# Kernel optimization log

Hardware: AMD Instinct MI355X
Metric: run time of the kernel (lower is better)

## Reference

```python
import jax, jax.numpy as jnp
import numpy as np

H = 256      # hidden_size
IN = 128     # lstm input_size
A = 64       # attention_features
F = 1024     # vocab_features
V = 50000    # vocab_size
S = 512      # src_len
T = 32       # dec_len
B = 32       # batch


def _lstm_layer(x, h0, c0, Wih, Whh, bih, bhh):
    # x: [T,B,in]; PyTorch gate order i,f,g,o
    def step(carry, xt):
        h, c = carry
        g = xt @ Wih.T + h @ Whh.T + (bih + bhh)          # [B,4H]
        i, f, gg, o = jnp.split(g, 4, axis=-1)
        c = jax.nn.sigmoid(f) * c + jax.nn.sigmoid(i) * jnp.tanh(gg)
        h = jax.nn.sigmoid(o) * jnp.tanh(c)
        return (h, c), h
    (hT, cT), ys = jax.lax.scan(step, (h0, c0), x)
    return ys, hT, cT


def setup_inputs() -> dict:
    key = jax.random.key(0)
    ks = jax.random.split(key, 24)
    sc = 0.05
    d = {
        "output_enc": jax.random.normal(ks[0], (S, B, 2 * H), jnp.float32),
        "input_dec": jax.random.normal(ks[1], (T, B, IN), jnp.float32),
        "hidden_enc": jax.random.normal(ks[2], (4, B, H), jnp.float32),
        "cell_state_enc": jax.random.normal(ks[3], (4, B, H), jnp.float32),
        "att_mask": jnp.zeros((S, B, 1), jnp.float32),
        # LSTM layer 0 / 1 params
        "W_ih0": jax.random.normal(ks[4], (4 * H, IN)) * sc,
        "W_hh0": jax.random.normal(ks[5], (4 * H, H)) * sc,
        "b_ih0": jax.random.normal(ks[6], (4 * H,)) * sc,
        "b_hh0": jax.random.normal(ks[7], (4 * H,)) * sc,
        "W_ih1": jax.random.normal(ks[8], (4 * H, H)) * sc,
        "W_hh1": jax.random.normal(ks[9], (4 * H, H)) * sc,
        "b_ih1": jax.random.normal(ks[10], (4 * H,)) * sc,
        "b_hh1": jax.random.normal(ks[11], (4 * H,)) * sc,
        # reduce_dim: Linear(2H -> H)
        "W_red": jax.random.normal(ks[12], (H, 2 * H)) * sc,
        "b_red": jax.random.normal(ks[13], (H,)) * sc,
        # attention: Linear(3H+1 -> A), attn_out: Linear(A -> 1, no bias)
        "W_att": jax.random.normal(ks[14], (A, 3 * H + 1)) * sc,
        "b_att": jax.random.normal(ks[15], (A,)) * sc,
        "W_attout": jax.random.normal(ks[16], (1, A)) * sc,
        # vocab MLP: Linear(3H -> F), Linear(F -> V)
        "W_v1": jax.random.normal(ks[17], (F, 3 * H)) * sc,
        "b_v1": jax.random.normal(ks[18], (F,)) * sc,
        "W_v2": jax.random.normal(ks[19], (V, F)) * sc,
        "b_v2": jax.random.normal(ks[20], (V,)) * sc,
    }
    return d


def reference(output_enc, input_dec, hidden_enc, cell_state_enc, att_mask,
              W_ih0, W_hh0, b_ih0, b_hh0, W_ih1, W_hh1, b_ih1, b_hh1,
              W_red, b_red, W_att, b_att, W_attout, W_v1, b_v1, W_v2, b_v2):
    # first_word=True path: fold the 4 bidirectional encoder states into 2 layer states
    old_enc = jnp.concatenate([hidden_enc[0:2], hidden_enc[2:]], axis=-1)    # [2,B,2H]
    old_cell = jnp.concatenate([cell_state_enc[0:2], cell_state_enc[2:]], axis=-1)
    new_enc = old_enc @ W_red.T + b_red                                      # [2,B,H]
    new_cell = old_cell @ W_red.T + b_red

    # 2-layer unidirectional LSTM decoder
    y0, h0, c0 = _lstm_layer(input_dec, new_enc[0], new_cell[0], W_ih0, W_hh0, b_ih0, b_hh0)
    output_dec, h1, c1 = _lstm_layer(y0, new_enc[1], new_cell[1], W_ih1, W_hh1, b_ih1, b_hh1)
    hidden_dec = jnp.stack([h0, h1])
    cell_dec = jnp.stack([c0, c1])

    # split attention weight columns: concat([enc 2H | dec H | cov 1]) @ W_att.T
    Wa_enc = W_att[:, :2 * H]
    Wa_dec = W_att[:, 2 * H:3 * H]
    Wa_cov = W_att[:, 3 * H:]
    enc_proj = output_enc @ Wa_enc.T + b_att                                  # [S,B,A], hoisted

    cov0 = jnp.zeros(output_enc.shape[:2] + (1,), output_enc.dtype)           # [S,B,1]

    def step(coverage, dec_t):
        # dec_t: [B,H]
        e = jnp.tanh(enc_proj + dec_t @ Wa_dec.T + coverage @ Wa_cov.T)       # [S,B,A]
        e = e @ W_attout.T + att_mask                                          # [S,B,1]
        attn = jax.nn.softmax(e, axis=0)
        cov_loss = jnp.sum(jnp.minimum(attn, coverage), axis=0)               # [B,1]
        new_cov = coverage + attn
        context = jnp.sum(attn * output_enc, axis=0)                          # [B,2H]
        pv_in = jnp.concatenate([dec_t, context], axis=-1)                    # [B,3H]
        pv = (pv_in @ W_v1.T + b_v1) @ W_v2.T + b_v2                          # [B,V]
        return new_cov, (pv, cov_loss)

    _, (pvocab, coverage_loss) = jax.lax.scan(step, cov0, output_dec)
    return pvocab, coverage_loss, hidden_dec, cell_dec
```

## Files before the change

### kernel.cpp

```cpp
#include <hip/hip_runtime.h>
#include <hip/hip_bf16.h>
#include <cstddef>

#define H_    256
#define INP_  128
#define A_    64
#define F_    1024
#define V_    50000
#define S_    512
#define T_    32
#define B_    32
#define G4_   1024

typedef __attribute__((ext_vector_type(8))) _Float16 f16x8;
typedef __attribute__((ext_vector_type(4))) _Float16 f16x4;
typedef __attribute__((ext_vector_type(4))) float f32x4;

__device__ __forceinline__ float sigm_f(float x) { return 1.f / (1.f + __expf(-x)); }
__device__ __forceinline__ float tanh_f(float x) { float e = __expf(2.f * x); return 1.f - 2.f / (e + 1.f); }

__device__ __forceinline__ float wred_max(float v) {
#pragma unroll
    for (int o = 1; o < 64; o <<= 1) v = fmaxf(v, __shfl_xor(v, o));
    return v;
}
__device__ __forceinline__ float wred_sum(float v) {
#pragma unroll
    for (int o = 1; o < 64; o <<= 1) v += __shfl_xor(v, o);
    return v;
}

__device__ __forceinline__ void glds16(const void* g, void* l) {
    __builtin_amdgcn_global_load_lds((const __attribute__((address_space(1))) unsigned int*)g,
                                     (__attribute__((address_space(3))) unsigned int*)l, 16, 0, 0);
}

__global__ __launch_bounds__(256) void k_transpose_whh(const float* __restrict__ W0,
                                                       const float* __restrict__ W1,
                                                       float* __restrict__ T0,
                                                       float* __restrict__ T1) {
    int idx = blockIdx.x * 256 + threadIdx.x;
    int layer = idx >> 18;
    int i = idx & 262143;
    int k = i >> 10;
    int r = i & 1023;
    const float* W = layer ? W1 : W0;
    float* Tp = layer ? T1 : T0;
    Tp[i] = W[r * H_ + k];
}

__global__ __launch_bounds__(256) void k_reduce(const float* __restrict__ hid,
                                                const float* __restrict__ cel,
                                                const float* __restrict__ Wred,
                                                const float* __restrict__ bred,
                                                float* __restrict__ ne,
                                                float* __restrict__ nc) {
    int idx = blockIdx.x * 256 + threadIdx.x;
    int arr = idx >> 14;
    int rem = idx & 16383;
    int l = rem >> 13;
    int b = (rem >> 8) & 31;
    int j = rem & 255;
    const float* src = arr ? cel : hid;
    const float* w = Wred + j * 512;
    const float* s0 = src + (l * B_ + b) * H_;
    const float* s1 = src + ((l + 2) * B_ + b) * H_;
    float acc = bred[j];
#pragma unroll 8
    for (int d = 0; d < 256; ++d) acc += s0[d] * w[d];
#pragma unroll 8
    for (int d = 0; d < 256; ++d) acc += s1[d] * w[256 + d];
    float* dst = arr ? nc : ne;
    dst[l * (B_ * H_) + b * H_ + j] = acc;
}

__global__ __launch_bounds__(256) void k_gemm64(const float* __restrict__ A, int lda,
                                                const float* __restrict__ Bm, int ldb,
                                                const float* __restrict__ bias1,
                                                const float* __restrict__ bias2,
                                                float* __restrict__ C, int ldc, int K) {
    __shared__ float As[32 * 65];
    __shared__ float Bs[32 * 65];
    int tid = threadIdx.x;
    int m0 = blockIdx.x * 64, n0 = blockIdx.y * 64;
    int mym = (tid >> 4) * 4, myn = (tid & 15) * 4;
    float c[4][4] = {};
    for (int k0 = 0; k0 < K; k0 += 32) {
        __syncthreads();
#pragma unroll
        for (int p = 0; p < 8; ++p) {
            int idx = tid + p * 256;
            int k = idx & 31, m = idx >> 5;
            As[k * 65 + m] = A[(size_t)(m0 + m) * lda + k0 + k];
            Bs[k * 65 + m] = Bm[(size_t)(n0 + m) * ldb + k0 + k];
        }
        __syncthreads();
#pragma unroll
        for (int k = 0; k < 32; ++k) {
            float a0 = As[k * 65 + mym + 0];
            float a1 = As[k * 65 + mym + 1];
            float a2 = As[k * 65 + mym + 2];
            float a3 = As[k * 65 + mym + 3];
            float b0 = Bs[k * 65 + myn + 0];
            float b1 = Bs[k * 65 + myn + 1];
            float b2 = Bs[k * 65 + myn + 2];
            float b3 = Bs[k * 65 + myn + 3];
            c[0][0] += a0 * b0; c[0][1] += a0 * b1; c[0][2] += a0 * b2; c[0][3] += a0 * b3;
            c[1][0] += a1 * b0; c[1][1] += a1 * b1; c[1][2] += a1 * b2; c[1][3] += a1 * b3;
            c[2][0] += a2 * b0; c[2][1] += a2 * b1; c[2][2] += a2 * b2; c[2][3] += a2 * b3;
            c[3][0] += a3 * b0; c[3][1] += a3 * b1; c[3][2] += a3 * b2; c[3][3] += a3 * b3;
        }
    }
    float bj[4];
#pragma unroll
    for (int j = 0; j < 4; ++j) {
        int n = n0 + myn + j;
        bj[j] = (bias1 ? bias1[n] : 0.f) + (bias2 ? bias2[n] : 0.f);
    }
#pragma unroll
    for (int i = 0; i < 4; ++i) {
        size_t off = (size_t)(m0 + mym + i) * ldc + n0 + myn;
#pragma unroll
        for (int j = 0; j < 4; ++j) C[off + j] = c[i][j] + bj[j];
    }
}

__global__ __launch_bounds__(1024) void k_lstm(const float* __restrict__ gx,
                                               const float* __restrict__ WT,
                                               const float* __restrict__ h0,
                                               const float* __restrict__ c0,
                                               float* __restrict__ y, int ldy,
                                               float* __restrict__ outh,
                                               float* __restrict__ outc) {
    int b = blockIdx.x, tid = threadIdx.x;
    __shared__ float h_s[256], c_s[256], g_s[1024];
    if (tid < 256) { h_s[tid] = h0[b * H_ + tid]; c_s[tid] = c0[b * H_ + tid]; }
    __syncthreads();
    for (int t = 0; t < T_; ++t) {
        float base = gx[(size_t)(t * B_ + b) * G4_ + tid];
        const float* wp = WT + tid;
        float a0 = 0.f, a1 = 0.f, a2 = 0.f, a3 = 0.f;
#pragma unroll 2
        for (int k = 0; k < 256; k += 4) {
            a0 += wp[(size_t)(k + 0) * G4_] * h_s[k + 0];
            a1 += wp[(size_t)(k + 1) * G4_] * h_s[k + 1];
            a2 += wp[(size_t)(k + 2) * G4_] * h_s[k + 2];
            a3 += wp[(size_t)(k + 3) * G4_] * h_s[k + 3];
        }
        g_s[tid] = base + (a0 + a1) + (a2 + a3);
        __syncthreads();
        if (tid < 256) {
            float ii = sigm_f(g_s[tid]);
            float ff = sigm_f(g_s[256 + tid]);
            float gg = tanh_f(g_s[512 + tid]);
            float oo = sigm_f(g_s[768 + tid]);
            float cc = ff * c_s[tid] + ii * gg;
            float hh = oo * tanh_f(cc);
            c_s[tid] = cc; h_s[tid] = hh;
            y[(size_t)(t * B_ + b) * ldy + tid] = hh;
        }
        __syncthreads();
    }
    if (tid < 256) { outh[b * H_ + tid] = h_s[tid]; outc[b * H_ + tid] = c_s[tid]; }
}

__global__ __launch_bounds__(512) void k_att_scan(const float* __restrict__ encp,
                                                  const float* __restrict__ decp,
                                                  const float* __restrict__ Watt,
                                                  const float* __restrict__ Wout,
                                                  const float* __restrict__ mask,
                                                  float* __restrict__ attn_ws,
                                                  float* __restrict__ covloss_out) {
    int b = blockIdx.x, s = threadIdx.x;
    __shared__ float dp[64], wcov[64], wo[64], red[8];
    float ep[64];
    const float* ebase = encp + ((size_t)s * B_ + b) * A_;
#pragma unroll
    for (int a4 = 0; a4 < 16; ++a4) {
        float4 v = reinterpret_cast<const float4*>(ebase)[a4];
        ep[a4 * 4 + 0] = v.x; ep[a4 * 4 + 1] = v.y; ep[a4 * 4 + 2] = v.z; ep[a4 * 4 + 3] = v.w;
    }
    float msk = mask[s * B_ + b];
    float cov = 0.f;
    if (s < 64) { wcov[s] = Watt[s * 769 + 768]; wo[s] = Wout[s]; }
    __syncthreads();
    for (int t = 0; t < T_; ++t) {
        if (s < 64) dp[s] = decp[(t * B_ + b) * A_ + s];
        __syncthreads();
        float sc = 0.f;
#pragma unroll 8
        for (int a = 0; a < 64; ++a) sc += tanh_f(ep[a] + dp[a] + cov * wcov[a]) * wo[a];
        sc += msk;
        float mx = wred_max(sc);
        if ((s & 63) == 0) red[s >> 6] = mx;
        __syncthreads();
        mx = fmaxf(fmaxf(fmaxf(red[0], red[1]), fmaxf(red[2], red[3])),
                   fmaxf(fmaxf(red[4], red[5]), fmaxf(red[6], red[7])));
        float p = __expf(sc - mx);
        float su = wred_sum(p);
        __syncthreads();
        if ((s & 63) == 0) red[s >> 6] = su;
        __syncthreads();
        su = (red[0] + red[1]) + (red[2] + red[3]) + (red[4] + red[5]) + (red[6] + red[7]);
        float at = p / su;
        float cl = wred_sum(fminf(at, cov));
        __syncthreads();
        if ((s & 63) == 0) red[s >> 6] = cl;
        __syncthreads();
        if (s == 0)
            covloss_out[t * B_ + b] = (red[0] + red[1]) + (red[2] + red[3]) + (red[4] + red[5]) + (red[6] + red[7]);
        attn_ws[((size_t)b * T_ + t) * S_ + s] = at;
        cov += at;
        __syncthreads();
    }
}

__global__ __launch_bounds__(256) void k_att_ctx(const float* __restrict__ enc,
                                                 const float* __restrict__ attn_ws,
                                                 float* __restrict__ pvin) {
    int b = blockIdx.x >> 2, dt = blockIdx.x & 3;
    int tid = threadIdx.x;
    __shared__ float ats[32 * 33];
    __shared__ float es[32 * 132];
    int ti = tid >> 5;
    int dj = tid & 31;
    float c[4][4] = {};
    for (int s0 = 0; s0 < S_; s0 += 32) {
        __syncthreads();
#pragma unroll
        for (int p = 0; p < 4; ++p) {
            int q = tid + p * 256;
            int tt = q >> 5, ss = q & 31;
            ats[tt * 33 + ss] = attn_ws[((size_t)b * T_ + tt) * S_ + s0 + ss];
        }
#pragma unroll
        for (int p = 0; p < 4; ++p) {
            int q = tid + p * 256;
            int ss = q >> 5, c4 = q & 31;
            float4 v = *reinterpret_cast<const float4*>(enc + (size_t)(s0 + ss) * (B_ * 512) + b * 512 + dt * 128 + c4 * 4);
            *reinterpret_cast<float4*>(&es[ss * 132 + c4 * 4]) = v;
        }
        __syncthreads();
#pragma unroll 4
        for (int s2 = 0; s2 < 32; ++s2) {
            float4 bv = *reinterpret_cast<const float4*>(&es[s2 * 132 + dj * 4]);
            float a0 = ats[(ti * 4 + 0) * 33 + s2];
            float a1 = ats[(ti * 4 + 1) * 33 + s2];
            float a2 = ats[(ti * 4 + 2) * 33 + s2];
            float a3 = ats[(ti * 4 + 3) * 33 + s2];
            c[0][0] += a0 * bv.x; c[0][1] += a0 * bv.y; c[0][2] += a0 * bv.z; c[0][3] += a0 * bv.w;
            c[1][0] += a1 * bv.x; c[1][1] += a1 * bv.y; c[1][2] += a1 * bv.z; c[1][3] += a1 * bv.w;
            c[2][0] += a2 * bv.x; c[2][1] += a2 * bv.y; c[2][2] += a2 * bv.z; c[2][3] += a2 * bv.w;
            c[3][0] += a3 * bv.x; c[3][1] += a3 * bv.y; c[3][2] += a3 * bv.z; c[3][3] += a3 * bv.w;
        }
    }
#pragma unroll
    for (int u = 0; u < 4; ++u) {
        int t = ti * 4 + u;
        float4 o = {c[u][0], c[u][1], c[u][2], c[u][3]};
        *reinterpret_cast<float4*>(pvin + (size_t)(t * B_ + b) * 768 + 256 + dt * 128 + dj * 4) = o;
    }
}

__global__ __launch_bounds__(256) void k_convert_h1(const float* __restrict__ h1,
                                                    _Float16* __restrict__ hf) {
    int i = (blockIdx.x * 256 + threadIdx.x) * 4;
    float4 v = *reinterpret_cast<const float4*>(h1 + i);
    f16x4 o = {(_Float16)v.x, (_Float16)v.y, (_Float16)v.z, (_Float16)v.w};
    *reinterpret_cast<f16x4*>(hf + i) = o;
}

__global__ __launch_bounds__(256, 2) void k_pvocab2(const _Float16* __restrict__ h1f,
                                                    const float* __restrict__ w2,
                                                    const float* __restrict__ bias,
                                                    float* __restrict__ C) {
    __shared__ _Float16 As[2][128 * 32];
    __shared__ _Float16 Bs[2][128 * 32];
    int tid = threadIdx.x;
    int lane = tid & 63, w = tid >> 6;
    int d = blockIdx.x;
    int xd = d & 7, c = d >> 3;
    int mtile = c & 7;
    int ntile = ((c >> 3) << 3) + xd;
    int m0 = mtile * 128, n0 = ntile * 128;
    int wm = w >> 1, wn = w & 1;
    int l15 = lane & 15, lq = lane >> 4;

    int L0 = (w * 2) * 64 + lane;
    int L1 = L0 + 64;
    int am0 = L0 >> 2, as0 = L0 & 3;
    int am1 = L1 >> 2, as1 = L1 & 3;
    int ac0 = as0 ^ ((am0 >> 1) & 3);
    int ac1 = as1 ^ ((am1 >> 1) & 3);
    const _Float16* ag0 = h1f + (size_t)(m0 + am0) * 1024 + ac0 * 8;
    const _Float16* ag1 = h1f + (size_t)(m0 + am1) * 1024 + ac1 * 8;
    int adst0 = (w * 2) * 512;
    int adst1 = adst0 + 512;

    int br = tid >> 1, bhf = tid & 1;
    bool bok = (n0 + br) < V_;
    const float* bg = w2 + (size_t)(n0 + br) * 1024 + bhf * 16;
    int bsw = (br >> 1) & 3;
    int bo0 = br * 32 + ((bhf * 2) ^ bsw) * 8;
    int bo1 = br * 32 + ((bhf * 2 + 1) ^ bsw) * 8;

    int aoff[4], boff[4];
#pragma unroll
    for (int mt = 0; mt < 4; ++mt) {
        int row = wm * 64 + mt * 16 + l15;
        aoff[mt] = row * 32 + ((lq ^ ((row >> 1) & 3)) * 8);
    }
#pragma unroll
    for (int nt = 0; nt < 4; ++nt) {
        int row = wn * 64 + nt * 16 + l15;
        boff[nt] = row * 32 + ((lq ^ ((row >> 1) & 3)) * 8);
    }

    f32x4 acc[4][4];
#pragma unroll
    for (int i = 0; i < 4; ++i)
#pragma unroll
        for (int j = 0; j < 4; ++j) acc[i][j] = (f32x4){0.f, 0.f, 0.f, 0.f};

    float4 bv0, bv1, bv2, bv3;
    glds16(ag0, &As[0][adst0]);
    glds16(ag1, &As[0][adst1]);
    if (bok) {
        bv0 = *reinterpret_cast<const float4*>(bg + 0);
        bv1 = *reinterpret_cast<const float4*>(bg + 4);
        bv2 = *reinterpret_cast<const float4*>(bg + 8);
        bv3 = *reinterpret_cast<const float4*>(bg + 12);
    } else {
        bv0 = bv1 = bv2 = bv3 = make_float4(0.f, 0.f, 0.f, 0.f);
    }
    {
        f16x8 c0 = {(_Float16)bv0.x, (_Float16)bv0.y, (_Float16)bv0.z, (_Float16)bv0.w,
                    (_Float16)bv1.x, (_Float16)bv1.y, (_Float16)bv1.z, (_Float16)bv1.w};
        f16x8 c1 = {(_Float16)bv2.x, (_Float16)bv2.y, (_Float16)bv2.z, (_Float16)bv2.w,
                    (_Float16)bv3.x, (_Float16)bv3.y, (_Float16)bv3.z, (_Float16)bv3.w};
        *reinterpret_cast<f16x8*>(&Bs[0][bo0]) = c0;
        *reinterpret_cast<f16x8*>(&Bs[0][bo1]) = c1;
    }
    __syncthreads();

    for (int kt = 0; kt < 32; ++kt) {
        int cur = kt & 1, nxt = cur ^ 1;
        if (kt < 31) {
            int k1 = (kt + 1) * 32;
            glds16(ag0 + k1, &As[nxt][adst0]);
            glds16(ag1 + k1, &As[nxt][adst1]);
            if (bok) {
                bv0 = *reinterpret_cast<const float4*>(bg + k1 + 0);
                bv1 = *reinterpret_cast<const float4*>(bg + k1 + 4);
                bv2 = *reinterpret_cast<const float4*>(bg + k1 + 8);
                bv3 = *reinterpret_cast<const float4*>(bg + k1 + 12);
            }
        }
        f16x8 af[4], bf[4];
#pragma unroll
        for (int mt = 0; mt < 4; ++mt) af[mt] = *reinterpret_cast<const f16x8*>(&As[cur][aoff[mt]]);
#pragma unroll
        for (int nt = 0; nt < 4; ++nt) bf[nt] = *reinterpret_cast<const f16x8*>(&Bs[cur][boff[nt]]);
#pragma unroll
        for (int mt = 0; mt < 4; ++mt)
#pragma unroll
            for (int nt = 0; nt < 4; ++nt)
                acc[mt][nt] = __builtin_amdgcn_mfma_f32_16x16x32_f16(af[mt], bf[nt], acc[mt][nt], 0, 0, 0);
        if (kt < 31) {
            f16x8 c0 = {(_Float16)bv0.x, (_Float16)bv0.y, (_Float16)bv0.z, (_Float16)bv0.w,
                        (_Float16)bv1.x, (_Float16)bv1.y, (_Float16)bv1.z, (_Float16)bv1.w};
            f16x8 c1 = {(_Float16)bv2.x, (_Float16)bv2.y, (_Float16)bv2.z, (_Float16)bv2.w,
                        (_Float16)bv3.x, (_Float16)bv3.y, (_Float16)bv3.z, (_Float16)bv3.w};
            *reinterpret_cast<f16x8*>(&Bs[nxt][bo0]) = c0;
            *reinterpret_cast<f16x8*>(&Bs[nxt][bo1]) = c1;
        }
        __syncthreads();
    }

#pragma unroll
    for (int nt = 0; nt < 4; ++nt) {
        int n = n0 + wn * 64 + nt * 16 + l15;
        if (n < V_) {
            float bb = bias[n];
#pragma unroll
            for (int mt = 0; mt < 4; ++mt) {
                int mbase = m0 + wm * 64 + mt * 16 + lq * 4;
#pragma unroll
                for (int rr = 0; rr < 4; ++rr)
                    C[(size_t)(mbase + rr) * V_ + n] = acc[mt][nt][rr] + bb;
            }
        }
    }
}

extern "C" void kernel_launch(void* const* d_in, const int* in_sizes, int n_in,
                              void* d_out, int out_size, void* d_ws, size_t ws_size,
                              hipStream_t stream) {
    const float* output_enc = (const float*)d_in[0];
    const float* input_dec  = (const float*)d_in[1];
    const float* hidden_enc = (const float*)d_in[2];
    const float* cell_enc   = (const float*)d_in[3];
    const float* att_mask   = (const float*)d_in[4];
    const float* W_ih0 = (const float*)d_in[5];
    const float* W_hh0 = (const float*)d_in[6];
    const float* b_ih0 = (const float*)d_in[7];
    const float* b_hh0 = (const float*)d_in[8];
    const float* W_ih1 = (const float*)d_in[9];
    const float* W_hh1 = (const float*)d_in[10];
    const float* b_ih1 = (const float*)d_in[11];
    const float* b_hh1 = (const float*)d_in[12];
    const float* W_red = (const float*)d_in[13];
    const float* b_red = (const float*)d_in[14];
    const float* W_att = (const float*)d_in[15];
    const float* b_att = (const float*)d_in[16];
    const float* W_attout = (const float*)d_in[17];
    const float* W_v1 = (const float*)d_in[18];
    const float* b_v1 = (const float*)d_in[19];
    const float* W_v2 = (const float*)d_in[20];
    const float* b_v2 = (const float*)d_in[21];
    float* out = (float*)d_out;
    float* ws  = (float*)d_ws;

    float* WT0     = ws;
    float* WT1     = WT0 + 262144;
    float* newenc  = WT1 + 262144;
    float* newcell = newenc + 16384;
    float* gx0     = newcell + 16384;
    float* gx1     = gx0 + 1048576;
    float* y0      = gx1 + 1048576;
    float* pvin    = y0 + 262144;
    float* encp    = pvin + 786432;
    float* decp    = encp + 1048576;
    float* h1      = decp + 65536;
    float* attn    = h1 + 1048576;
    _Float16* h1f  = (_Float16*)gx0;

    float* out_pv = out;
    float* out_cl = out + 51200000;
    float* out_h  = out + 51201024;
    float* out_c  = out + 51217408;

    k_transpose_whh<<<2048, 256, 0, stream>>>(W_hh0, W_hh1, WT0, WT1);
    k_reduce<<<128, 256, 0, stream>>>(hidden_enc, cell_enc, W_red, b_red, newenc, newcell);
    k_gemm64<<<dim3(16, 16), 256, 0, stream>>>(input_dec, 128, W_ih0, 128, b_ih0, b_hh0, gx0, 1024, 128);
    k_gemm64<<<dim3(256, 1), 256, 0, stream>>>(output_enc, 512, W_att, 769, b_att, nullptr, encp, 64, 512);
    k_lstm<<<32, 1024, 0, stream>>>(gx0, WT0, newenc, newcell, y0, 256, out_h, out_c);
    k_gemm64<<<dim3(16, 16), 256, 0, stream>>>(y0, 256, W_ih1, 256, b_ih1, b_hh1, gx1, 1024, 256);
    k_lstm<<<32, 1024, 0, stream>>>(gx1, WT1, newenc + 8192, newcell + 8192, pvin, 768, out_h + 8192, out_c + 8192);
    k_gemm64<<<dim3(16, 1), 256, 0, stream>>>(pvin, 768, W_att + 512, 769, nullptr, nullptr, decp, 64, 256);
    k_att_scan<<<32, 512, 0, stream>>>(encp, decp, W_att, W_attout, att_mask, attn, out_cl);
    k_att_ctx<<<128, 256, 0, stream>>>(output_enc, attn, pvin);
    k_gemm64<<<dim3(16, 16), 256, 0, stream>>>(pvin, 768, W_v1, 768, b_v1, nullptr, h1, 1024, 768);
    k_convert_h1<<<1024, 256, 0, stream>>>(h1, h1f);
    k_pvocab2<<<3136, 256, 0, stream>>>(h1f, W_v2, b_v2, out_pv);
}
```

Measured before the change: 1.568 ms.

## Fuse both LSTM layers into a persistent wavefront kernel and enlarge vocab GEMM tiles

Replaces the two sequential per-batch LSTM kernels with one persistent 64-block kernel. It keeps packed recurrent and input weights in LDS and runs layer 1 one step behind layer 0, with a software grid barrier between steps. The encoder-state reduction becomes a gather plus a tiled GEMM, and the vocab first-layer GEMM writes fp16 directly instead of running a separate conversion kernel. The vocab projection uses 256x128 tiles with 512 threads, so each W_v2 row is loaded once per two batch tiles. The grid barrier assumes all 64 blocks are co-resident and adds a global sync per timestep.

```diff
diff --git a/kernel.cpp b/kernel.cpp
--- a/kernel.cpp
+++ b/kernel.cpp
@@ -11,6 +11,7 @@
 #define T_    32
 #define B_    32
 #define G4_   1024
+#define NB_LSTM 64
 
 typedef __attribute__((ext_vector_type(8))) _Float16 f16x8;
 typedef __attribute__((ext_vector_type(4))) _Float16 f16x4;
@@ -35,43 +36,51 @@
                                      (__attribute__((address_space(3))) unsigned int*)l, 16, 0, 0);
 }
 
-__global__ __launch_bounds__(256) void k_transpose_whh(const float* __restrict__ W0,
-                                                       const float* __restrict__ W1,
-                                                       float* __restrict__ T0,
-                                                       float* __restrict__ T1) {
+__device__ __forceinline__ void gsync(int* cnt, int* gen, int target, int nb) {
+    __syncthreads();
+    if (threadIdx.x == 0) {
+        __threadfence();
+        int v = __hip_atomic_fetch_add(cnt, 1, __ATOMIC_ACQ_REL, __HIP_MEMORY_SCOPE_AGENT);
+        if (v == nb - 1) {
+            __hip_atomic_store(cnt, 0, __ATOMIC_RELEASE, __HIP_MEMORY_SCOPE_AGENT);
+            __hip_atomic_fetch_add(gen, 1, __ATOMIC_ACQ_REL, __HIP_MEMORY_SCOPE_AGENT);
+        } else {
+            while (__hip_atomic_load(gen, __ATOMIC_ACQUIRE, __HIP_MEMORY_SCOPE_AGENT) < target) {
+                __builtin_amdgcn_s_sleep(2);
+            }
+        }
+        __threadfence();
+    }
+    __syncthreads();
+}
+
+__global__ __launch_bounds__(256) void k_pack(const float* __restrict__ Whh0,
+                                              const float* __restrict__ Whh1,
+                                              const float* __restrict__ Wih1,
+                                              float* __restrict__ Wpk,
+                                              int* __restrict__ sync) {
+    if (blockIdx.x == 0 && threadIdx.x < 2) sync[threadIdx.x] = 0;
     int idx = blockIdx.x * 256 + threadIdx.x;
-    int layer = idx >> 18;
-    int i = idx & 262143;
-    int k = i >> 10;
-    int r = i & 1023;
-    const float* W = layer ? W1 : W0;
-    float* Tp = layer ? T1 : T0;
-    Tp[i] = W[r * H_ + k];
-}
-
-__global__ __launch_bounds__(256) void k_reduce(const float* __restrict__ hid,
+    int k = idx & 255;
+    int r = (idx >> 8) & 15;
+    int bk = (idx >> 12) & 63;
+    int seg = idx >> 18;
+    int cl = r >> 2, g = r & 3;
+    int srow = g * 256 + bk * 4 + cl;
+    const float* W = seg == 0 ? Whh0 : (seg == 1 ? Whh1 : Wih1);
+    Wpk[idx] = W[srow * 256 + k];
+}
+
+__global__ __launch_bounds__(256) void k_gather(const float* __restrict__ hid,
                                                 const float* __restrict__ cel,
-                                                const float* __restrict__ Wred,
-                                                const float* __restrict__ bred,
-                                                float* __restrict__ ne,
-                                                float* __restrict__ nc) {
+                                                float* __restrict__ Ared) {
     int idx = blockIdx.x * 256 + threadIdx.x;
-    int arr = idx >> 14;
-    int rem = idx & 16383;
-    int l = rem >> 13;
-    int b = (rem >> 8) & 31;
-    int j = rem & 255;
+    int d = idx & 511;
+    int r = idx >> 9;
+    int arr = r >> 6, l = (r >> 5) & 1, b = r & 31;
     const float* src = arr ? cel : hid;
-    const float* w = Wred + j * 512;
-    const float* s0 = src + (l * B_ + b) * H_;
-    const float* s1 = src + ((l + 2) * B_ + b) * H_;
-    float acc = bred[j];
-#pragma unroll 8
-    for (int d = 0; d < 256; ++d) acc += s0[d] * w[d];
-#pragma unroll 8
-    for (int d = 0; d < 256; ++d) acc += s1[d] * w[256 + d];
-    float* dst = arr ? nc : ne;
-    dst[l * (B_ * H_) + b * H_ + j] = acc;
+    int lay = l + ((d >> 8) << 1);
+    Ared[idx] = src[(lay * 32 + b) * 256 + (d & 255)];
 }
 
 __global__ __launch_bounds__(256) void k_gemm64(const float* __restrict__ A, int lda,
@@ -125,43 +134,155 @@
     }
 }
 
-__global__ __launch_bounds__(1024) void k_lstm(const float* __restrict__ gx,
-                                               const float* __restrict__ WT,
-                                               const float* __restrict__ h0,
-                                               const float* __restrict__ c0,
-                                               float* __restrict__ y, int ldy,
+__global__ __launch_bounds__(256) void k_gemm64h(const float* __restrict__ A, int lda,
+                                                 const float* __restrict__ Bm, int ldb,
+                                                 const float* __restrict__ bias1,
+                                                 _Float16* __restrict__ C16, int ldc, int K) {
+    __shared__ float As[32 * 65];
+    __shared__ float Bs[32 * 65];
+    int tid = threadIdx.x;
+    int m0 = blockIdx.x * 64, n0 = blockIdx.y * 64;
+    int mym = (tid >> 4) * 4, myn = (tid & 15) * 4;
+    float c[4][4] = {};
+    for (int k0 = 0; k0 < K; k0 += 32) {
+        __syncthreads();
+#pragma unroll
+        for (int p = 0; p < 8; ++p) {
+            int idx = tid + p * 256;
+            int k = idx & 31, m = idx >> 5;
+            As[k * 65 + m] = A[(size_t)(m0 + m) * lda + k0 + k];
+            Bs[k * 65 + m] = Bm[(size_t)(n0 + m) * ldb + k0 + k];
+        }
+        __syncthreads();
+#pragma unroll
+        for (int k = 0; k < 32; ++k) {
+            float a0 = As[k * 65 + mym + 0];
+            float a1 = As[k * 65 + mym + 1];
+            float a2 = As[k * 65 + mym + 2];
+            float a3 = As[k * 65 + mym + 3];
+            float b0 = Bs[k * 65 + myn + 0];
+            float b1 = Bs[k * 65 + myn + 1];
+            float b2 = Bs[k * 65 + myn + 2];
+            float b3 = Bs[k * 65 + myn + 3];
+            c[0][0] += a0 * b0; c[0][1] += a0 * b1; c[0][2] += a0 * b2; c[0][3] += a0 * b3;
+            c[1][0] += a1 * b0; c[1][1] += a1 * b1; c[1][2] += a1 * b2; c[1][3] += a1 * b3;
+            c[2][0] += a2 * b0; c[2][1] += a2 * b1; c[2][2] += a2 * b2; c[2][3] += a2 * b3;
+            c[3][0] += a3 * b0; c[3][1] += a3 * b1; c[3][2] += a3 * b2; c[3][3] += a3 * b3;
+        }
+    }
+    float bj[4];
+#pragma unroll
+    for (int j = 0; j < 4; ++j) bj[j] = bias1[n0 + myn + j];
+#pragma unroll
+    for (int i = 0; i < 4; ++i) {
+        size_t off = (size_t)(m0 + mym + i) * ldc + n0 + myn;
+        f16x4 o = {(_Float16)(c[i][0] + bj[0]), (_Float16)(c[i][1] + bj[1]),
+                   (_Float16)(c[i][2] + bj[2]), (_Float16)(c[i][3] + bj[3])};
+        *reinterpret_cast<f16x4*>(C16 + off) = o;
+    }
+}
+
+__global__ __launch_bounds__(512) void k_lstm2(const float* __restrict__ gx0,
+                                               const float* __restrict__ Wpk,
+                                               const float* __restrict__ newenc,
+                                               const float* __restrict__ newcell,
+                                               const float* __restrict__ bih1,
+                                               const float* __restrict__ bhh1,
+                                               float* __restrict__ h0g,
+                                               float* __restrict__ h1g,
+                                               float* __restrict__ pvin,
                                                float* __restrict__ outh,
-                                               float* __restrict__ outc) {
-    int b = blockIdx.x, tid = threadIdx.x;
-    __shared__ float h_s[256], c_s[256], g_s[1024];
-    if (tid < 256) { h_s[tid] = h0[b * H_ + tid]; c_s[tid] = c0[b * H_ + tid]; }
-    __syncthreads();
-    for (int t = 0; t < T_; ++t) {
-        float base = gx[(size_t)(t * B_ + b) * G4_ + tid];
-        const float* wp = WT + tid;
-        float a0 = 0.f, a1 = 0.f, a2 = 0.f, a3 = 0.f;
-#pragma unroll 2
-        for (int k = 0; k < 256; k += 4) {
-            a0 += wp[(size_t)(k + 0) * G4_] * h_s[k + 0];
-            a1 += wp[(size_t)(k + 1) * G4_] * h_s[k + 1];
-            a2 += wp[(size_t)(k + 2) * G4_] * h_s[k + 2];
-            a3 += wp[(size_t)(k + 3) * G4_] * h_s[k + 3];
-        }
-        g_s[tid] = base + (a0 + a1) + (a2 + a3);
-        __syncthreads();
-        if (tid < 256) {
-            float ii = sigm_f(g_s[tid]);
-            float ff = sigm_f(g_s[256 + tid]);
-            float gg = tanh_f(g_s[512 + tid]);
-            float oo = sigm_f(g_s[768 + tid]);
-            float cc = ff * c_s[tid] + ii * gg;
-            float hh = oo * tanh_f(cc);
-            c_s[tid] = cc; h_s[tid] = hh;
-            y[(size_t)(t * B_ + b) * ldy + tid] = hh;
-        }
-        __syncthreads();
-    }
-    if (tid < 256) { outh[b * H_ + tid] = h_s[tid]; outc[b * H_ + tid] = c_s[tid]; }
+                                               float* __restrict__ outc,
+                                               int* __restrict__ scnt,
+                                               int* __restrict__ sgen) {
+    __shared__ float W0s[16][260], W1h[16][260], W1i[16][260];
+    __shared__ float bufA[32][260], bufB[32][260];
+    int tid = threadIdx.x, bk = blockIdx.x;
+    int b = tid >> 4, cl = (tid >> 2) & 3, g = tid & 3;
+    int r = cl * 4 + g;
+    int cellg = bk * 4 + cl;
+    int row_w = g * 256 + cellg;
+    for (int i = tid; i < 16 * 256; i += 512) {
+        int rr = i >> 8, kk = i & 255;
+        W0s[rr][kk] = Wpk[((0 * 64 + bk) * 16 + rr) * 256 + kk];
+        W1h[rr][kk] = Wpk[((1 * 64 + bk) * 16 + rr) * 256 + kk];
+        W1i[rr][kk] = Wpk[((2 * 64 + bk) * 16 + rr) * 256 + kk];
+    }
+    float bs1 = bih1[row_w] + bhh1[row_w];
+    float c0 = newcell[b * 256 + cellg];
+    float c1 = newcell[8192 + b * 256 + cellg];
+    for (int i = tid; i < 8192; i += 512) {
+        h0g[8192 + i] = newenc[i];
+        h1g[8192 + i] = newenc[8192 + i];
+    }
+    gsync(scnt, sgen, 1, NB_LSTM);
+    int lq4 = (tid & 63) & ~3;
+    int sb = tid >> 4, sk = (tid & 15) * 16;
+    for (int s = 0; s <= 32; ++s) {
+        const float* srcA = h0g + (((s + 1) & 1) << 13);
+        const float* srcB = h1g + ((s & 1) << 13);
+#pragma unroll
+        for (int u = 0; u < 16; u += 4) {
+            *reinterpret_cast<float4*>(&bufA[sb][sk + u]) =
+                *reinterpret_cast<const float4*>(srcA + sb * 256 + sk + u);
+            *reinterpret_cast<float4*>(&bufB[sb][sk + u]) =
+                *reinterpret_cast<const float4*>(srcB + sb * 256 + sk + u);
+        }
+        __syncthreads();
+        if (s < 32) {
+            float acc = gx0[(size_t)(s * 32 + b) * 1024 + row_w];
+            float a0 = 0.f, a1 = 0.f, a2 = 0.f, a3 = 0.f;
+#pragma unroll 8
+            for (int k = 0; k < 256; k += 4) {
+                float4 wv = *reinterpret_cast<const float4*>(&W0s[r][k]);
+                float4 hv = *reinterpret_cast<const float4*>(&bufA[b][k]);
+                a0 = fmaf(wv.x, hv.x, a0); a1 = fmaf(wv.y, hv.y, a1);
+                a2 = fmaf(wv.z, hv.z, a2); a3 = fmaf(wv.w, hv.w, a3);
+            }
+            acc += (a0 + a1) + (a2 + a3);
+            float ii = __shfl(acc, lq4 + 0);
+            float ff = __shfl(acc, lq4 + 1);
+            float gg = __shfl(acc, lq4 + 2);
+            float oo = __shfl(acc, lq4 + 3);
+            c0 = sigm_f(ff) * c0 + sigm_f(ii) * tanh_f(gg);
+            float h = sigm_f(oo) * tanh_f(c0);
+            if (g == 0) {
+                h0g[((s & 1) << 13) + b * 256 + cellg] = h;
+                if (s == 31) outh[b * 256 + cellg] = h;
+            }
+            if (g == 1 && s == 31) outc[b * 256 + cellg] = c0;
+        }
+        if (s >= 1) {
+            float acc = bs1;
+            float a0 = 0.f, a1 = 0.f, a2 = 0.f, a3 = 0.f;
+#pragma unroll 4
+            for (int k = 0; k < 256; k += 4) {
+                float4 wi = *reinterpret_cast<const float4*>(&W1i[r][k]);
+                float4 ya = *reinterpret_cast<const float4*>(&bufA[b][k]);
+                float4 wh = *reinterpret_cast<const float4*>(&W1h[r][k]);
+                float4 hb = *reinterpret_cast<const float4*>(&bufB[b][k]);
+                a0 = fmaf(wi.x, ya.x, a0); a1 = fmaf(wi.y, ya.y, a1);
+                a2 = fmaf(wi.z, ya.z, a2); a3 = fmaf(wi.w, ya.w, a3);
+                a0 = fmaf(wh.x, hb.x, a0); a1 = fmaf(wh.y, hb.y, a1);
+                a2 = fmaf(wh.z, hb.z, a2); a3 = fmaf(wh.w, hb.w, a3);
+            }
+            acc += (a0 + a1) + (a2 + a3);
+            float ii = __shfl(acc, lq4 + 0);
+            float ff = __shfl(acc, lq4 + 1);
+            float gg = __shfl(acc, lq4 + 2);
+            float oo = __shfl(acc, lq4 + 3);
+            c1 = sigm_f(ff) * c1 + sigm_f(ii) * tanh_f(gg);
+            float h = sigm_f(oo) * tanh_f(c1);
+            int t1 = s - 1;
+            if (g == 0) {
+                h1g[((t1 & 1) << 13) + b * 256 + cellg] = h;
+                pvin[(size_t)(t1 * 32 + b) * 768 + cellg] = h;
+                if (t1 == 31) outh[8192 + b * 256 + cellg] = h;
+            }
+            if (g == 1 && t1 == 31) outc[8192 + b * 256 + cellg] = c1;
+        }
+        gsync(scnt, sgen, s + 2, NB_LSTM);
+    }
 }
 
 __global__ __launch_bounds__(512) void k_att_scan(const float* __restrict__ encp,
@@ -262,47 +383,33 @@
     }
 }
 
-__global__ __launch_bounds__(256) void k_convert_h1(const float* __restrict__ h1,
-                                                    _Float16* __restrict__ hf) {
-    int i = (blockIdx.x * 256 + threadIdx.x) * 4;
-    float4 v = *reinterpret_cast<const float4*>(h1 + i);
-    f16x4 o = {(_Float16)v.x, (_Float16)v.y, (_Float16)v.z, (_Float16)v.w};
-    *reinterpret_cast<f16x4*>(hf + i) = o;
-}
-
-__global__ __launch_bounds__(256, 2) void k_pvocab2(const _Float16* __restrict__ h1f,
+__global__ __launch_bounds__(512, 4) void k_pvocab3(const _Float16* __restrict__ h1f,
                                                     const float* __restrict__ w2,
                                                     const float* __restrict__ bias,
                                                     float* __restrict__ C) {
-    __shared__ _Float16 As[2][128 * 32];
+    __shared__ _Float16 As[2][256 * 32];
     __shared__ _Float16 Bs[2][128 * 32];
     int tid = threadIdx.x;
     int lane = tid & 63, w = tid >> 6;
     int d = blockIdx.x;
     int xd = d & 7, c = d >> 3;
-    int mtile = c & 7;
-    int ntile = ((c >> 3) << 3) + xd;
-    int m0 = mtile * 128, n0 = ntile * 128;
+    int mtile = c & 3;
+    int ntile = (c >> 2) * 8 + xd;
+    int m0 = mtile * 256, n0 = ntile * 128;
     int wm = w >> 1, wn = w & 1;
     int l15 = lane & 15, lq = lane >> 4;
 
-    int L0 = (w * 2) * 64 + lane;
-    int L1 = L0 + 64;
-    int am0 = L0 >> 2, as0 = L0 & 3;
-    int am1 = L1 >> 2, as1 = L1 & 3;
-    int ac0 = as0 ^ ((am0 >> 1) & 3);
-    int ac1 = as1 ^ ((am1 >> 1) & 3);
-    const _Float16* ag0 = h1f + (size_t)(m0 + am0) * 1024 + ac0 * 8;
-    const _Float16* ag1 = h1f + (size_t)(m0 + am1) * 1024 + ac1 * 8;
-    int adst0 = (w * 2) * 512;
-    int adst1 = adst0 + 512;
-
-    int br = tid >> 1, bhf = tid & 1;
+    int q0 = w * 128 + lane, q1 = q0 + 64;
+    int ar0 = q0 >> 2, ac0 = (q0 & 3) ^ ((ar0 >> 1) & 3);
+    int ar1 = q1 >> 2, ac1 = (q1 & 3) ^ ((ar1 >> 1) & 3);
+    const _Float16* ag0 = h1f + (size_t)(m0 + ar0) * 1024 + ac0 * 8;
+    const _Float16* ag1 = h1f + (size_t)(m0 + ar1) * 1024 + ac1 * 8;
+    int adst0 = q0 * 8, adst1 = q1 * 8;
+
+    int br = tid >> 2, bch = tid & 3;
+    int bo = br * 32 + ((bch ^ ((br >> 1) & 3)) * 8);
     bool bok = (n0 + br) < V_;
-    const float* bg = w2 + (size_t)(n0 + br) * 1024 + bhf * 16;
-    int bsw = (br >> 1) & 3;
-    int bo0 = br * 32 + ((bhf * 2) ^ bsw) * 8;
-    int bo1 = br * 32 + ((bhf * 2 + 1) ^ bsw) * 8;
+    const float* bg = w2 + (size_t)(n0 + br) * 1024 + bch * 8;
 
     int aoff[4], boff[4];
 #pragma unroll
@@ -322,24 +429,19 @@
 #pragma unroll
         for (int j = 0; j < 4; ++j) acc[i][j] = (f32x4){0.f, 0.f, 0.f, 0.f};
 
-    float4 bv0, bv1, bv2, bv3;
+    float4 bv0, bv1;
     glds16(ag0, &As[0][adst0]);
     glds16(ag1, &As[0][adst1]);
     if (bok) {
         bv0 = *reinterpret_cast<const float4*>(bg + 0);
         bv1 = *reinterpret_cast<const float4*>(bg + 4);
-        bv2 = *reinterpret_cast<const float4*>(bg + 8);
-        bv3 = *reinterpret_cast<const float4*>(bg + 12);
     } else {
-        bv0 = bv1 = bv2 = bv3 = make_float4(0.f, 0.f, 0.f, 0.f);
+        bv0 = bv1 = make_float4(0.f, 0.f, 0.f, 0.f);
     }
     {
         f16x8 c0 = {(_Float16)bv0.x, (_Float16)bv0.y, (_Float16)bv0.z, (_Float16)bv0.w,
                     (_Float16)bv1.x, (_Float16)bv1.y, (_Float16)bv1.z, (_Float16)bv1.w};
-        f16x8 c1 = {(_Float16)bv2.x, (_Float16)bv2.y, (_Float16)bv2.z, (_Float16)bv2.w,
-                    (_Float16)bv3.x, (_Float16)bv3.y, (_Float16)bv3.z, (_Float16)bv3.w};
-        *reinterpret_cast<f16x8*>(&Bs[0][bo0]) = c0;
-        *reinterpret_cast<f16x8*>(&Bs[0][bo1]) = c1;
+        *reinterpret_cast<f16x8*>(&Bs[0][bo]) = c0;
     }
     __syncthreads();
 
@@ -352,8 +454,6 @@
             if (bok) {
                 bv0 = *reinterpret_cast<const float4*>(bg + k1 + 0);
                 bv1 = *reinterpret_cast<const float4*>(bg + k1 + 4);
-                bv2 = *reinterpret_cast<const float4*>(bg + k1 + 8);
-                bv3 = *reinterpret_cast<const float4*>(bg + k1 + 12);
             }
         }
         f16x8 af[4], bf[4];
@@ -369,10 +469,7 @@
         if (kt < 31) {
             f16x8 c0 = {(_Float16)bv0.x, (_Float16)bv0.y, (_Float16)bv0.z, (_Float16)bv0.w,
                         (_Float16)bv1.x, (_Float16)bv1.y, (_Float16)bv1.z, (_Float16)bv1.w};
-            f16x8 c1 = {(_Float16)bv2.x, (_Float16)bv2.y, (_Float16)bv2.z, (_Float16)bv2.w,
-                        (_Float16)bv3.x, (_Float16)bv3.y, (_Float16)bv3.z, (_Float16)bv3.w};
-            *reinterpret_cast<f16x8*>(&Bs[nxt][bo0]) = c0;
-            *reinterpret_cast<f16x8*>(&Bs[nxt][bo1]) = c1;
+            *reinterpret_cast<f16x8*>(&Bs[nxt][bo]) = c0;
         }
         __syncthreads();
     }
@@ -421,36 +518,35 @@
     float* out = (float*)d_out;
     float* ws  = (float*)d_ws;
 
-    float* WT0     = ws;
-    float* WT1     = WT0 + 262144;
-    float* newenc  = WT1 + 262144;
+    float* Wpk     = ws;
+    float* Ared    = Wpk + 786432;
+    float* newenc  = Ared + 65536;
     float* newcell = newenc + 16384;
     float* gx0     = newcell + 16384;
-    float* gx1     = gx0 + 1048576;
-    float* y0      = gx1 + 1048576;
-    float* pvin    = y0 + 262144;
+    float* h0g     = gx0 + 1048576;
+    float* h1g     = h0g + 16384;
+    float* pvin    = h1g + 16384;
     float* encp    = pvin + 786432;
     float* decp    = encp + 1048576;
-    float* h1      = decp + 65536;
-    float* attn    = h1 + 1048576;
-    _Float16* h1f  = (_Float16*)gx0;
+    float* attn    = decp + 65536;
+    _Float16* h1f  = (_Float16*)(attn + 524288);
+    int* sync      = (int*)(attn + 524288 + 524288);
 
     float* out_pv = out;
     float* out_cl = out + 51200000;
     float* out_h  = out + 51201024;
     float* out_c  = out + 51217408;
 
-    k_transpose_whh<<<2048, 256, 0, stream>>>(W_hh0, W_hh1, WT0, WT1);
-    k_reduce<<<128, 256, 0, stream>>>(hidden_enc, cell_enc, W_red, b_red, newenc, newcell);
+    k_pack<<<3072, 256, 0, stream>>>(W_hh0, W_hh1, W_ih1, Wpk, sync);
+    k_gather<<<256, 256, 0, stream>>>(hidden_enc, cell_enc, Ared);
+    k_gemm64<<<dim3(2, 4), 256, 0, stream>>>(Ared, 512, W_red, 512, b_red, nullptr, newenc, 256, 512);
     k_gemm64<<<dim3(16, 16), 256, 0, stream>>>(input_dec, 128, W_ih0, 128, b_ih0, b_hh0, gx0, 1024, 128);
     k_gemm64<<<dim3(256, 1), 256, 0, stream>>>(output_enc, 512, W_att, 769, b_att, nullptr, encp, 64, 512);
-    k_lstm<<<32, 1024, 0, stream>>>(gx0, WT0, newenc, newcell, y0, 256, out_h, out_c);
-    k_gemm64<<<dim3(16, 16), 256, 0, stream>>>(y0, 256, W_ih1, 256, b_ih1, b_hh1, gx1, 1024, 256);
-    k_lstm<<<32, 1024, 0, stream>>>(gx1, WT1, newenc + 8192, newcell + 8192, pvin, 768, out_h + 8192, out_c + 8192);
+    k_lstm2<<<NB_LSTM, 512, 0, stream>>>(gx0, Wpk, newenc, newcell, b_ih1, b_hh1,
+                                         h0g, h1g, pvin, out_h, out_c, sync, sync + 1);
     k_gemm64<<<dim3(16, 1), 256, 0, stream>>>(pvin, 768, W_att + 512, 769, nullptr, nullptr, decp, 64, 256);
     k_att_scan<<<32, 512, 0, stream>>>(encp, decp, W_att, W_attout, att_mask, attn, out_cl);
     k_att_ctx<<<128, 256, 0, stream>>>(output_enc, attn, pvin);
-    k_gemm64<<<dim3(16, 16), 256, 0, stream>>>(pvin, 768, W_v1, 768, b_v1, nullptr, h1, 1024, 768);
-    k_convert_h1<<<1024, 256, 0, stream>>>(h1, h1f);
-    k_pvocab2<<<3136, 256, 0, stream>>>(h1f, W_v2, b_v2, out_pv);
-}
+    k_gemm64h<<<dim3(16, 16), 256, 0, stream>>>(pvin, 768, W_v1, 768, b_v1, h1f, 1024, 768);
+    k_pvocab3<<<1568, 512, 0, stream>>>(h1f, W_v2, b_v2, out_pv);
+}
```

Result: faster. 1.473 ms (-6.1%).
